# Optimization experiments

Hardware: AMD Instinct MI355X
Metric: run time of the kernel (lower is better)

## Reference

```python
import jax, jax.numpy as jnp
import numpy as np

EPSILON = 1e-5
N_ITER = 100  # module uses 100 iterations in eval mode (5 in training)
R = 0.01


def mdot(x, y):
    # Minkowski inner product with metric diag(-1, 1, ..., 1), reduced over dim 1.
    return jnp.sum(x * y, axis=1, keepdims=True) - 2.0 * x[:, :1] * y[:, :1]


def mnorm(x):
    return jnp.sqrt(jnp.abs(mdot(x, x)))


def arccosh(x):
    x = jnp.clip(x, 1.0 + EPSILON, None)
    return jnp.log(x) + jnp.log1p(jnp.sqrt(x * x - 1.0) / x)


def setup_inputs() -> dict:
    key = jax.random.key(0)
    data = jax.random.normal(key, (131072, 512), dtype=jnp.float32)
    return {"data": data}


def reference(data):
    # project onto hyperboloid: time coordinate sqrt(1 + |x|^2)
    t = jnp.sqrt(1.0 + jnp.sum(data * data, axis=1, keepdims=True))
    projected = jnp.concatenate([t, data], axis=1)  # [N, d+1]

    mean = jnp.mean(projected, axis=0, keepdims=True)  # [1, d+1]
    mean = mean / mnorm(mean)

    def step(mean, _):
        # log_map(mean, projected), broadcasting mean over N
        d = arccosh(-mdot(mean, projected))               # [N, 1]
        logm = d / jnp.sinh(d) * (projected - jnp.cosh(d) * mean)  # [N, d+1]
        g = -2.0 * jnp.mean(logm, axis=0, keepdims=True)  # [1, d+1]
        y = -R * g
        n = jnp.clip(mnorm(y), EPSILON, None)
        mean = jnp.cosh(n) * mean + jnp.sinh(n) / n * y   # exp_map
        mean = mean / mnorm(mean)
        return mean, None

    mean, _ = jax.lax.scan(step, mean, None, length=N_ITER)
    return jnp.squeeze(mean)[1:]  # drop time coordinate -> [d]
```

## Files before the change

### kernel.cpp

```cpp
#include <hip/hip_runtime.h>
#include <hip/hip_fp16.h>
#include <math.h>
#include <cstddef>

#define N_PTS 131072
#define SDIM  512
#define D1    513

static constexpr int NITER = 100;
static constexpr int BLK   = 512;
static constexpr int GRID  = 512;
static constexpr int WPB   = BLK / 64;
static constexpr int NW    = GRID * WPB;
static constexpr int NPAIR = N_PTS / 2;
static constexpr int PPW   = NPAIR / NW;

struct Ws {
  double colsum[514];
  double part[514][GRID];
  float  meanbuf[2][516];
  float  t_tab[N_PTS];
};

__device__ __forceinline__ float2 cvt2(unsigned u) {
  union { unsigned u; __half2 h; } c; c.u = u; return __half22float2(c.h);
}
__device__ __forceinline__ unsigned pack2(float a, float b) {
  union { unsigned u; __half2 h; } c; c.h = __floats2half2_rn(a, b); return c.u;
}

template<bool INIT>
__device__ __forceinline__ void compute_mean(const Ws* __restrict__ ws,
                                             const float* __restrict__ mprev,
                                             int l, float out[9])
{
  double sv[9];
  #pragma unroll
  for (int q = 0; q < 9; ++q) {
    int c = q * 64 + l;
    sv[q] = (c < D1) ? ws->colsum[c] : 0.0;
  }

  if constexpr (INIT) {
    double r[9]; double s2 = 0.0;
    #pragma unroll
    for (int q = 0; q < 9; ++q) {
      int c = q * 64 + l;
      r[q] = (c < D1) ? sv[q] / (double)N_PTS : 0.0;
      s2 += r[q] * r[q];
    }
    #pragma unroll
    for (int m = 1; m < 64; m <<= 1) s2 += __shfl_xor(s2, m);
    double rt = __shfl(r[8], 0);
    double inv = 1.0 / sqrt(fabs(s2 - 2.0 * rt * rt));
    #pragma unroll
    for (int q = 0; q < 9; ++q) out[q] = (float)(r[q] * inv);
  } else {
    double cc = ws->colsum[513];
    double mv[9], yv[9]; double sy = 0.0;
    #pragma unroll
    for (int q = 0; q < 9; ++q) {
      int c = q * 64 + l;
      mv[q] = 0.0; yv[q] = 0.0;
      if (c < D1) {
        double m = (double)mprev[c];
        double y = 0.02 * (sv[q] - cc * m) / (double)N_PTS;
        mv[q] = m; yv[q] = y;
        sy += y * y;
      }
    }
    #pragma unroll
    for (int m = 1; m < 64; m <<= 1) sy += __shfl_xor(sy, m);
    double yt = __shfl(yv[8], 0);
    double n = sqrt(fabs(sy - 2.0 * yt * yt));
    n = fmax(n, 1e-5);
    double ch = cosh(n);
    double sn = (n < 1e-4) ? (1.0 + n * n / 6.0) : (sinh(n) / n);
    double nm[9]; double s2 = 0.0;
    #pragma unroll
    for (int q = 0; q < 9; ++q) {
      nm[q] = ch * mv[q] + sn * yv[q];
      s2 += nm[q] * nm[q];
    }
    #pragma unroll
    for (int m = 1; m < 64; m <<= 1) s2 += __shfl_xor(s2, m);
    double nt = __shfl(nm[8], 0);
    double inv = 1.0 / sqrt(fabs(s2 - 2.0 * nt * nt));
    #pragma unroll
    for (int q = 0; q < 9; ++q) out[q] = (float)(nm[q] * inv);
  }
}

__global__ __launch_bounds__(BLK, 4)
void init_kernel(const float* __restrict__ data, __half* __restrict__ hdata,
                 Ws* __restrict__ ws)
{
  const int l    = threadIdx.x & 63;
  const int sl   = l & 31;
  const int half = l >> 5;
  const int wid  = threadIdx.x >> 6;
  const int gw   = blockIdx.x * WPB + wid;

  float accf[16] = {};
  double acc_t = 0.0;

  const int p0 = gw * PPW;

  float4 v0, v1, v2, v3, n0, n1, n2, n3;
  {
    const float4* f4 = (const float4*)(data + (size_t)(2 * p0 + half) * SDIM);
    v0 = f4[2*sl]; v1 = f4[2*sl+1]; v2 = f4[64+2*sl]; v3 = f4[64+2*sl+1];
  }

  for (int k = 0; k < PPW; ++k) {
    if (k + 1 < PPW) {
      const float4* f4 = (const float4*)(data + (size_t)(2 * (p0 + k + 1) + half) * SDIM);
      n0 = f4[2*sl]; n1 = f4[2*sl+1]; n2 = f4[64+2*sl]; n3 = f4[64+2*sl+1];
    } else { n0 = v0; n1 = v1; n2 = v2; n3 = v3; }

    const int row = 2 * (p0 + k) + half;

    {
      uint4 ua, ub;
      ua.x = pack2(v0.x, v0.y); ua.y = pack2(v0.z, v0.w);
      ua.z = pack2(v1.x, v1.y); ua.w = pack2(v1.z, v1.w);
      ub.x = pack2(v2.x, v2.y); ub.y = pack2(v2.z, v2.w);
      ub.z = pack2(v3.x, v3.y); ub.w = pack2(v3.z, v3.w);
      uint4* hb = (uint4*)(hdata + (size_t)row * SDIM);
      hb[sl] = ua; hb[32 + sl] = ub;
    }

    float sqa = v0.x * v0.x;
    sqa = fmaf(v0.y, v0.y, sqa); sqa = fmaf(v0.z, v0.z, sqa); sqa = fmaf(v0.w, v0.w, sqa);
    sqa = fmaf(v1.x, v1.x, sqa); sqa = fmaf(v1.y, v1.y, sqa);
    sqa = fmaf(v1.z, v1.z, sqa); sqa = fmaf(v1.w, v1.w, sqa);
    float sqb = v2.x * v2.x;
    sqb = fmaf(v2.y, v2.y, sqb); sqb = fmaf(v2.z, v2.z, sqb); sqb = fmaf(v2.w, v2.w, sqb);
    sqb = fmaf(v3.x, v3.x, sqb); sqb = fmaf(v3.y, v3.y, sqb);
    sqb = fmaf(v3.z, v3.z, sqb); sqb = fmaf(v3.w, v3.w, sqb);
    float sq = sqa + sqb;
    #pragma unroll
    for (int m = 1; m < 32; m <<= 1) sq += __shfl_xor(sq, m);

    float t = sqrtf(1.0f + sq);
    if (sl == 0) { ws->t_tab[row] = t; acc_t += (double)t; }

    accf[0]  += v0.x; accf[1]  += v0.y; accf[2]  += v0.z; accf[3]  += v0.w;
    accf[4]  += v1.x; accf[5]  += v1.y; accf[6]  += v1.z; accf[7]  += v1.w;
    accf[8]  += v2.x; accf[9]  += v2.y; accf[10] += v2.z; accf[11] += v2.w;
    accf[12] += v3.x; accf[13] += v3.y; accf[14] += v3.z; accf[15] += v3.w;

    v0 = n0; v1 = n1; v2 = n2; v3 = n3;
  }

  #pragma unroll
  for (int i = 0; i < 16; ++i) accf[i] += __shfl_xor(accf[i], 32);
  acc_t += __shfl_xor(acc_t, 32);

  __shared__ double s_red[WPB][514];
  if (half == 0) {
    #pragma unroll
    for (int i = 0; i < 8; ++i) {
      s_red[wid][8*sl + i]       = (double)accf[i];
      s_red[wid][256 + 8*sl + i] = (double)accf[8 + i];
    }
  }
  if (l == 0) { s_red[wid][512] = acc_t; s_red[wid][513] = 0.0; }
  __syncthreads();

  for (int c = threadIdx.x; c < 514; c += BLK) {
    double s = 0.0;
    #pragma unroll
    for (int w2 = 0; w2 < WPB; ++w2) s += s_red[w2][c];
    ws->part[c][blockIdx.x] = s;
  }
}

template<bool FIRST>
__global__ __launch_bounds__(BLK, 4)
void iter_kernel(const __half* __restrict__ hdata, Ws* __restrict__ ws,
                 const float* __restrict__ mprev, float* __restrict__ mnext)
{
  const int l    = threadIdx.x & 63;
  const int sl   = l & 31;
  const int half = l >> 5;
  const int wid  = threadIdx.x >> 6;
  const int gw   = blockIdx.x * WPB + wid;

  const int p0 = gw * PPW;

#define LDH(Ra, Rb, p) do {                                                   \
    const uint4* b_ = (const uint4*)(hdata + (size_t)(2 * (p) + half) * SDIM);\
    Ra = b_[sl]; Rb = b_[32 + sl];                                            \
  } while (0)

  uint4 Aa, Ab, Ba, Bb, Pa, Pb, Qa, Qb, Ra, Rb, Sa, Sb;
  LDH(Aa, Ab, p0 + 0);
  LDH(Ba, Bb, p0 + 1);

  __shared__ __align__(16) float s_mean[516];
  if (threadIdx.x < 64) {
    float outm[9];
    compute_mean<FIRST>(ws, mprev, threadIdx.x, outm);
    #pragma unroll
    for (int q = 0; q < 9; ++q) {
      int c = q * 64 + threadIdx.x;
      if (c < D1) {
        s_mean[c] = outm[q];
        if (blockIdx.x == 0) mnext[c] = outm[q];
      }
    }
  }
  __syncthreads();

  const float m0 = s_mean[512];
  const float4* mp4 = (const float4*)s_mean;
  const float4 mkA0 = mp4[2*sl],      mkA1 = mp4[2*sl + 1];
  const float4 mkB0 = mp4[64 + 2*sl], mkB1 = mp4[64 + 2*sl + 1];

  float accf[16] = {};
  double acc_t = 0.0, acc_cc = 0.0;
  const float* __restrict__ ttab = ws->t_tab;

  LDH(Pa, Pb, p0 + 2);
  LDH(Qa, Qb, p0 + 3);
  Ra = Aa; Rb = Ab; Sa = Ba; Sb = Bb;

  for (int kk = 0; kk < PPW; kk += 2) {
    if (kk + 4 < PPW) {
      LDH(Ra, Rb, p0 + kk + 4);
      LDH(Sa, Sb, p0 + kk + 5);
    }
    const float tA = ttab[2 * (p0 + kk)     + half];
    const float tB = ttab[2 * (p0 + kk + 1) + half];

    float2 f;
    f = cvt2(Aa.x); float dA  = f.x * mkA0.x;        dA  = fmaf(f.y, mkA0.y, dA);
    f = cvt2(Aa.y); dA  = fmaf(f.x, mkA0.z, dA);     dA  = fmaf(f.y, mkA0.w, dA);
    f = cvt2(Aa.z); dA  = fmaf(f.x, mkA1.x, dA);     dA  = fmaf(f.y, mkA1.y, dA);
    f = cvt2(Aa.w); dA  = fmaf(f.x, mkA1.z, dA);     dA  = fmaf(f.y, mkA1.w, dA);
    f = cvt2(Ab.x); float dA2 = f.x * mkB0.x;        dA2 = fmaf(f.y, mkB0.y, dA2);
    f = cvt2(Ab.y); dA2 = fmaf(f.x, mkB0.z, dA2);    dA2 = fmaf(f.y, mkB0.w, dA2);
    f = cvt2(Ab.z); dA2 = fmaf(f.x, mkB1.x, dA2);    dA2 = fmaf(f.y, mkB1.y, dA2);
    f = cvt2(Ab.w); dA2 = fmaf(f.x, mkB1.z, dA2);    dA2 = fmaf(f.y, mkB1.w, dA2);
    float dotA = dA + dA2;

    f = cvt2(Ba.x); float dB  = f.x * mkA0.x;        dB  = fmaf(f.y, mkA0.y, dB);
    f = cvt2(Ba.y); dB  = fmaf(f.x, mkA0.z, dB);     dB  = fmaf(f.y, mkA0.w, dB);
    f = cvt2(Ba.z); dB  = fmaf(f.x, mkA1.x, dB);     dB  = fmaf(f.y, mkA1.y, dB);
    f = cvt2(Ba.w); dB  = fmaf(f.x, mkA1.z, dB);     dB  = fmaf(f.y, mkA1.w, dB);
    f = cvt2(Bb.x); float dB2 = f.x * mkB0.x;        dB2 = fmaf(f.y, mkB0.y, dB2);
    f = cvt2(Bb.y); dB2 = fmaf(f.x, mkB0.z, dB2);    dB2 = fmaf(f.y, mkB0.w, dB2);
    f = cvt2(Bb.z); dB2 = fmaf(f.x, mkB1.x, dB2);    dB2 = fmaf(f.y, mkB1.y, dB2);
    f = cvt2(Bb.w); dB2 = fmaf(f.x, mkB1.z, dB2);    dB2 = fmaf(f.y, mkB1.w, dB2);
    float dotB = dB + dB2;

    #pragma unroll
    for (int m = 1; m < 32; m <<= 1) {
      dotA += __shfl_xor(dotA, m);
      dotB += __shfl_xor(dotB, m);
    }

    const float aA = fmaf(m0, tA, -dotA);
    const float aB = fmaf(m0, tB, -dotB);
    const float xA = fmaxf(aA, 1.0f + 1e-5f);
    const float xB = fmaxf(aB, 1.0f + 1e-5f);
    const float sA = sqrtf(fmaf(xA, xA, -1.0f));
    const float sB = sqrtf(fmaf(xB, xB, -1.0f));
    const float ddA = logf(xA + sA);
    const float ddB = logf(xB + sB);
    const float wA = ddA / sA;
    const float wB = ddB / sB;
    if (sl == 0) {
      acc_cc += fma((double)wA, (double)xA, (double)wB * (double)xB);
      acc_t  += fma((double)wA, (double)tA, (double)wB * (double)tB);
    }

    float2 a0, a1;
    a0 = cvt2(Aa.x); a1 = cvt2(Ba.x);
    accf[0]  = fmaf(wA, a0.x, fmaf(wB, a1.x, accf[0]));
    accf[1]  = fmaf(wA, a0.y, fmaf(wB, a1.y, accf[1]));
    a0 = cvt2(Aa.y); a1 = cvt2(Ba.y);
    accf[2]  = fmaf(wA, a0.x, fmaf(wB, a1.x, accf[2]));
    accf[3]  = fmaf(wA, a0.y, fmaf(wB, a1.y, accf[3]));
    a0 = cvt2(Aa.z); a1 = cvt2(Ba.z);
    accf[4]  = fmaf(wA, a0.x, fmaf(wB, a1.x, accf[4]));
    accf[5]  = fmaf(wA, a0.y, fmaf(wB, a1.y, accf[5]));
    a0 = cvt2(Aa.w); a1 = cvt2(Ba.w);
    accf[6]  = fmaf(wA, a0.x, fmaf(wB, a1.x, accf[6]));
    accf[7]  = fmaf(wA, a0.y, fmaf(wB, a1.y, accf[7]));
    a0 = cvt2(Ab.x); a1 = cvt2(Bb.x);
    accf[8]  = fmaf(wA, a0.x, fmaf(wB, a1.x, accf[8]));
    accf[9]  = fmaf(wA, a0.y, fmaf(wB, a1.y, accf[9]));
    a0 = cvt2(Ab.y); a1 = cvt2(Bb.y);
    accf[10] = fmaf(wA, a0.x, fmaf(wB, a1.x, accf[10]));
    accf[11] = fmaf(wA, a0.y, fmaf(wB, a1.y, accf[11]));
    a0 = cvt2(Ab.z); a1 = cvt2(Bb.z);
    accf[12] = fmaf(wA, a0.x, fmaf(wB, a1.x, accf[12]));
    accf[13] = fmaf(wA, a0.y, fmaf(wB, a1.y, accf[13]));
    a0 = cvt2(Ab.w); a1 = cvt2(Bb.w);
    accf[14] = fmaf(wA, a0.x, fmaf(wB, a1.x, accf[14]));
    accf[15] = fmaf(wA, a0.y, fmaf(wB, a1.y, accf[15]));

    Aa = Pa; Ab = Pb; Ba = Qa; Bb = Qb;
    Pa = Ra; Pb = Rb; Qa = Sa; Qb = Sb;
  }
#undef LDH

  #pragma unroll
  for (int i = 0; i < 16; ++i) accf[i] += __shfl_xor(accf[i], 32);
  acc_t  += __shfl_xor(acc_t, 32);
  acc_cc += __shfl_xor(acc_cc, 32);

  __shared__ double s_red[WPB][514];
  if (half == 0) {
    #pragma unroll
    for (int i = 0; i < 8; ++i) {
      s_red[wid][8*sl + i]       = (double)accf[i];
      s_red[wid][256 + 8*sl + i] = (double)accf[8 + i];
    }
  }
  if (l == 0) { s_red[wid][512] = acc_t; s_red[wid][513] = acc_cc; }
  __syncthreads();

  for (int c = threadIdx.x; c < 514; c += BLK) {
    double s = 0.0;
    #pragma unroll
    for (int w2 = 0; w2 < WPB; ++w2) s += s_red[w2][c];
    ws->part[c][blockIdx.x] = s;
  }
}

__global__ __launch_bounds__(64)
void colreduce_kernel(Ws* __restrict__ ws)
{
  const int c = blockIdx.x;
  const int l = threadIdx.x;
  const double* col = ws->part[c];
  double s = 0.0;
  #pragma unroll
  for (int k = 0; k < GRID / 64; ++k) s += col[l + 64 * k];
  #pragma unroll
  for (int m = 1; m < 64; m <<= 1) s += __shfl_xor(s, m);
  if (l == 0) ws->colsum[c] = s;
}

__global__ __launch_bounds__(64)
void final_kernel(Ws* __restrict__ ws, const float* __restrict__ mprev,
                  float* __restrict__ mnext)
{
  float outm[9];
  compute_mean<false>(ws, mprev, threadIdx.x, outm);
  #pragma unroll
  for (int q = 0; q < 9; ++q) {
    int c = q * 64 + threadIdx.x;
    if (c < D1) mnext[c] = outm[q];
  }
}

__global__ void write_out_kernel(const float* __restrict__ mean, float* __restrict__ out)
{
  int i = threadIdx.x;
  if (i < SDIM) out[i] = mean[i];
}

extern "C" void kernel_launch(void* const* d_in, const int* in_sizes, int n_in,
                              void* d_out, int out_size, void* d_ws, size_t ws_size,
                              hipStream_t stream)
{
  (void)in_sizes; (void)n_in; (void)out_size; (void)ws_size;
  const float* data = (const float*)d_in[0];
  Ws* ws = (Ws*)d_ws;

  const size_t hoff = (sizeof(Ws) + 255) & ~(size_t)255;
  __half* hdata = (__half*)((char*)d_ws + hoff);

  float* M0 = (float*)((char*)d_ws + offsetof(Ws, meanbuf));
  float* M1 = M0 + 516;

  init_kernel<<<dim3(GRID), dim3(BLK), 0, stream>>>(data, hdata, ws);
  colreduce_kernel<<<dim3(514), dim3(64), 0, stream>>>(ws);

  iter_kernel<true><<<dim3(GRID), dim3(BLK), 0, stream>>>(hdata, ws, M1, M0);
  colreduce_kernel<<<dim3(514), dim3(64), 0, stream>>>(ws);

  for (int it = 1; it < NITER; ++it) {
    const float* mp = (((it + 1) & 1) == 0) ? M0 : M1;
    float*       mn = ((it & 1) == 0) ? M0 : M1;
    iter_kernel<false><<<dim3(GRID), dim3(BLK), 0, stream>>>(hdata, ws, mp, mn);
    colreduce_kernel<<<dim3(514), dim3(64), 0, stream>>>(ws);
  }

  final_kernel<<<dim3(1), dim3(64), 0, stream>>>(ws, M1, M0);
  write_out_kernel<<<dim3(1), dim3(512), 0, stream>>>(M0, (float*)d_out);
}
```

Before: 3.180 ms.

## Store points as custom 8-bit floats and re-center weights around a constant

```diff
diff --git a/kernel.cpp b/kernel.cpp
--- a/kernel.cpp
+++ b/kernel.cpp
@@ -6,6 +6,7 @@
 #define N_PTS 131072
 #define SDIM  512
 #define D1    513
+#define W0F   0.169f
 
 static constexpr int NITER = 100;
 static constexpr int BLK   = 512;
@@ -17,16 +18,37 @@
 
 struct Ws {
   double colsum[514];
+  double X[514];
   double part[514][GRID];
   float  meanbuf[2][516];
   float  t_tab[N_PTS];
 };
 
-__device__ __forceinline__ float2 cvt2(unsigned u) {
-  union { unsigned u; __half2 h; } c; c.u = u; return __half22float2(c.h);
-}
-__device__ __forceinline__ unsigned pack2(float a, float b) {
-  union { unsigned u; __half2 h; } c; c.h = __floats2half2_rn(a, b); return c.u;
+__device__ __forceinline__ unsigned enc8(float x) {
+  unsigned u  = __float_as_uint(x);
+  unsigned s  = (u >> 24) & 0x80u;
+  unsigned au = u & 0x7fffffffu;
+  if (au < 0x3c800000u) return s;
+  unsigned r = au + 0x0007ffffu + ((au >> 20) & 1u);
+  unsigned e = r >> 23;
+  unsigned m = (r >> 20) & 7u;
+  if (e > 135u || (e == 135u && m > 6u)) return s | 0x7Eu;
+  return s | ((e - 120u) << 3) | m;
+}
+
+__device__ __forceinline__ unsigned dec8h(unsigned b) {
+  unsigned h = ((b & 0x80u) << 8) | ((b & 0x7fu) << 7);
+  return (b & 0x7fu) ? (h + 0x2000u) : h;
+}
+__device__ __forceinline__ float2 dec2(unsigned b0, unsigned b1) {
+  union { unsigned u; __half2 h; } c;
+  c.u = dec8h(b0) | (dec8h(b1) << 16);
+  return __half22float2(c.h);
+}
+__device__ __forceinline__ float4 dec4(unsigned v) {
+  float2 lo = dec2(v & 0xffu, (v >> 8) & 0xffu);
+  float2 hi = dec2((v >> 16) & 0xffu, v >> 24);
+  return make_float4(lo.x, lo.y, hi.x, hi.y);
 }
 
 template<bool INIT>
@@ -34,19 +56,12 @@
                                              const float* __restrict__ mprev,
                                              int l, float out[9])
 {
-  double sv[9];
-  #pragma unroll
-  for (int q = 0; q < 9; ++q) {
-    int c = q * 64 + l;
-    sv[q] = (c < D1) ? ws->colsum[c] : 0.0;
-  }
-
   if constexpr (INIT) {
     double r[9]; double s2 = 0.0;
     #pragma unroll
     for (int q = 0; q < 9; ++q) {
       int c = q * 64 + l;
-      r[q] = (c < D1) ? sv[q] / (double)N_PTS : 0.0;
+      r[q] = (c < D1) ? ws->colsum[c] / (double)N_PTS : 0.0;
       s2 += r[q] * r[q];
     }
     #pragma unroll
@@ -56,7 +71,28 @@
     #pragma unroll
     for (int q = 0; q < 9; ++q) out[q] = (float)(r[q] * inv);
   } else {
-    double cc = ws->colsum[513];
+    const double W0d = (double)W0F;
+    double xdm = 0.0;
+    #pragma unroll
+    for (int q = 0; q < 8; ++q) {
+      int c = q * 64 + l;
+      xdm += ws->X[c] * (double)mprev[c];
+    }
+    #pragma unroll
+    for (int m = 1; m < 64; m <<= 1) xdm += __shfl_xor(xdm, m);
+    const double T   = ws->X[512];
+    const double m0p = (double)mprev[512];
+
+    double sv[9];
+    #pragma unroll
+    for (int q = 0; q < 9; ++q) {
+      int c = q * 64 + l;
+      if (c < 512)       sv[q] = ws->colsum[c]   + W0d * ws->X[c];
+      else if (c == 512) sv[q] = ws->colsum[512] + W0d * T;
+      else               sv[q] = 0.0;
+    }
+    double cc = ws->colsum[513] + W0d * (m0p * T - xdm);
+
     double mv[9], yv[9]; double sy = 0.0;
     #pragma unroll
     for (int q = 0; q < 9; ++q) {
@@ -78,10 +114,7 @@
     double sn = (n < 1e-4) ? (1.0 + n * n / 6.0) : (sinh(n) / n);
     double nm[9]; double s2 = 0.0;
     #pragma unroll
-    for (int q = 0; q < 9; ++q) {
-      nm[q] = ch * mv[q] + sn * yv[q];
-      s2 += nm[q] * nm[q];
-    }
+    for (int q = 0; q < 9; ++q) { nm[q] = ch * mv[q] + sn * yv[q]; s2 += nm[q] * nm[q]; }
     #pragma unroll
     for (int m = 1; m < 64; m <<= 1) s2 += __shfl_xor(s2, m);
     double nt = __shfl(nm[8], 0);
@@ -92,7 +125,7 @@
 }
 
 __global__ __launch_bounds__(BLK, 4)
-void init_kernel(const float* __restrict__ data, __half* __restrict__ hdata,
+void init_kernel(const float* __restrict__ data, unsigned char* __restrict__ h8,
                  Ws* __restrict__ ws)
 {
   const int l    = threadIdx.x & 63;
@@ -103,7 +136,6 @@
 
   float accf[16] = {};
   double acc_t = 0.0;
-
   const int p0 = gw * PPW;
 
   float4 v0, v1, v2, v3, n0, n1, n2, n3;
@@ -121,13 +153,13 @@
     const int row = 2 * (p0 + k) + half;
 
     {
-      uint4 ua, ub;
-      ua.x = pack2(v0.x, v0.y); ua.y = pack2(v0.z, v0.w);
-      ua.z = pack2(v1.x, v1.y); ua.w = pack2(v1.z, v1.w);
-      ub.x = pack2(v2.x, v2.y); ub.y = pack2(v2.z, v2.w);
-      ub.z = pack2(v3.x, v3.y); ub.w = pack2(v3.z, v3.w);
-      uint4* hb = (uint4*)(hdata + (size_t)row * SDIM);
-      hb[sl] = ua; hb[32 + sl] = ub;
+      uint2 pa, pb;
+      pa.x = enc8(v0.x) | (enc8(v0.y) << 8) | (enc8(v0.z) << 16) | (enc8(v0.w) << 24);
+      pa.y = enc8(v1.x) | (enc8(v1.y) << 8) | (enc8(v1.z) << 16) | (enc8(v1.w) << 24);
+      pb.x = enc8(v2.x) | (enc8(v2.y) << 8) | (enc8(v2.z) << 16) | (enc8(v2.w) << 24);
+      pb.y = enc8(v3.x) | (enc8(v3.y) << 8) | (enc8(v3.z) << 16) | (enc8(v3.w) << 24);
+      uint2* hb = (uint2*)(h8 + (size_t)row * SDIM);
+      hb[sl] = pa; hb[32 + sl] = pb;
     }
 
     float sqa = v0.x * v0.x;
@@ -178,7 +210,7 @@
 
 template<bool FIRST>
 __global__ __launch_bounds__(BLK, 4)
-void iter_kernel(const __half* __restrict__ hdata, Ws* __restrict__ ws,
+void iter_kernel(const unsigned char* __restrict__ h8, Ws* __restrict__ ws,
                  const float* __restrict__ mprev, float* __restrict__ mnext)
 {
   const int l    = threadIdx.x & 63;
@@ -186,17 +218,16 @@
   const int half = l >> 5;
   const int wid  = threadIdx.x >> 6;
   const int gw   = blockIdx.x * WPB + wid;
-
-  const int p0 = gw * PPW;
-
-#define LDH(Ra, Rb, p) do {                                                   \
-    const uint4* b_ = (const uint4*)(hdata + (size_t)(2 * (p) + half) * SDIM);\
-    Ra = b_[sl]; Rb = b_[32 + sl];                                            \
+  const int p0   = gw * PPW;
+
+#define LDH8(R, p) do {                                                        \
+    const uint4* b_ = (const uint4*)(h8 + (size_t)(2 * (p) + half) * SDIM);    \
+    R = b_[sl];                                                                \
   } while (0)
 
-  uint4 Aa, Ab, Ba, Bb, Pa, Pb, Qa, Qb, Ra, Rb, Sa, Sb;
-  LDH(Aa, Ab, p0 + 0);
-  LDH(Ba, Bb, p0 + 1);
+  uint4 Aa, Ba, Pa, Qa, Ua, Va;
+  LDH8(Aa, p0 + 0);
+  LDH8(Ba, p0 + 1);
 
   __shared__ __align__(16) float s_mean[516];
   if (threadIdx.x < 64) {
@@ -215,44 +246,46 @@
 
   const float m0 = s_mean[512];
   const float4* mp4 = (const float4*)s_mean;
-  const float4 mkA0 = mp4[2*sl],      mkA1 = mp4[2*sl + 1];
-  const float4 mkB0 = mp4[64 + 2*sl], mkB1 = mp4[64 + 2*sl + 1];
+  const float4 mk0 = mp4[4*sl + 0], mk1 = mp4[4*sl + 1];
+  const float4 mk2 = mp4[4*sl + 2], mk3 = mp4[4*sl + 3];
 
   float accf[16] = {};
   double acc_t = 0.0, acc_cc = 0.0;
   const float* __restrict__ ttab = ws->t_tab;
 
-  LDH(Pa, Pb, p0 + 2);
-  LDH(Qa, Qb, p0 + 3);
-  Ra = Aa; Rb = Ab; Sa = Ba; Sb = Bb;
+  LDH8(Pa, p0 + 2);
+  LDH8(Qa, p0 + 3);
+  Ua = Aa; Va = Ba;
 
   for (int kk = 0; kk < PPW; kk += 2) {
     if (kk + 4 < PPW) {
-      LDH(Ra, Rb, p0 + kk + 4);
-      LDH(Sa, Sb, p0 + kk + 5);
+      LDH8(Ua, p0 + kk + 4);
+      LDH8(Va, p0 + kk + 5);
     }
     const float tA = ttab[2 * (p0 + kk)     + half];
     const float tB = ttab[2 * (p0 + kk + 1) + half];
 
-    float2 f;
-    f = cvt2(Aa.x); float dA  = f.x * mkA0.x;        dA  = fmaf(f.y, mkA0.y, dA);
-    f = cvt2(Aa.y); dA  = fmaf(f.x, mkA0.z, dA);     dA  = fmaf(f.y, mkA0.w, dA);
-    f = cvt2(Aa.z); dA  = fmaf(f.x, mkA1.x, dA);     dA  = fmaf(f.y, mkA1.y, dA);
-    f = cvt2(Aa.w); dA  = fmaf(f.x, mkA1.z, dA);     dA  = fmaf(f.y, mkA1.w, dA);
-    f = cvt2(Ab.x); float dA2 = f.x * mkB0.x;        dA2 = fmaf(f.y, mkB0.y, dA2);
-    f = cvt2(Ab.y); dA2 = fmaf(f.x, mkB0.z, dA2);    dA2 = fmaf(f.y, mkB0.w, dA2);
-    f = cvt2(Ab.z); dA2 = fmaf(f.x, mkB1.x, dA2);    dA2 = fmaf(f.y, mkB1.y, dA2);
-    f = cvt2(Ab.w); dA2 = fmaf(f.x, mkB1.z, dA2);    dA2 = fmaf(f.y, mkB1.w, dA2);
+    float4 a0 = dec4(Aa.x), a1 = dec4(Aa.y), a2 = dec4(Aa.z), a3 = dec4(Aa.w);
+    float4 b0 = dec4(Ba.x), b1 = dec4(Ba.y), b2 = dec4(Ba.z), b3 = dec4(Ba.w);
+
+    float dA = a0.x * mk0.x;
+    dA = fmaf(a0.y, mk0.y, dA); dA = fmaf(a0.z, mk0.z, dA); dA = fmaf(a0.w, mk0.w, dA);
+    dA = fmaf(a1.x, mk1.x, dA); dA = fmaf(a1.y, mk1.y, dA);
+    dA = fmaf(a1.z, mk1.z, dA); dA = fmaf(a1.w, mk1.w, dA);
+    float dA2 = a2.x * mk2.x;
+    dA2 = fmaf(a2.y, mk2.y, dA2); dA2 = fmaf(a2.z, mk2.z, dA2); dA2 = fmaf(a2.w, mk2.w, dA2);
+    dA2 = fmaf(a3.x, mk3.x, dA2); dA2 = fmaf(a3.y, mk3.y, dA2);
+    dA2 = fmaf(a3.z, mk3.z, dA2); dA2 = fmaf(a3.w, mk3.w, dA2);
     float dotA = dA + dA2;
 
-    f = cvt2(Ba.x); float dB  = f.x * mkA0.x;        dB  = fmaf(f.y, mkA0.y, dB);
-    f = cvt2(Ba.y); dB  = fmaf(f.x, mkA0.z, dB);     dB  = fmaf(f.y, mkA0.w, dB);
-    f = cvt2(Ba.z); dB  = fmaf(f.x, mkA1.x, dB);     dB  = fmaf(f.y, mkA1.y, dB);
-    f = cvt2(Ba.w); dB  = fmaf(f.x, mkA1.z, dB);     dB  = fmaf(f.y, mkA1.w, dB);
-    f = cvt2(Bb.x); float dB2 = f.x * mkB0.x;        dB2 = fmaf(f.y, mkB0.y, dB2);
-    f = cvt2(Bb.y); dB2 = fmaf(f.x, mkB0.z, dB2);    dB2 = fmaf(f.y, mkB0.w, dB2);
-    f = cvt2(Bb.z); dB2 = fmaf(f.x, mkB1.x, dB2);    dB2 = fmaf(f.y, mkB1.y, dB2);
-    f = cvt2(Bb.w); dB2 = fmaf(f.x, mkB1.z, dB2);    dB2 = fmaf(f.y, mkB1.w, dB2);
+    float dB = b0.x * mk0.x;
+    dB = fmaf(b0.y, mk0.y, dB); dB = fmaf(b0.z, mk0.z, dB); dB = fmaf(b0.w, mk0.w, dB);
+    dB = fmaf(b1.x, mk1.x, dB); dB = fmaf(b1.y, mk1.y, dB);
+    dB = fmaf(b1.z, mk1.z, dB); dB = fmaf(b1.w, mk1.w, dB);
+    float dB2 = b2.x * mk2.x;
+    dB2 = fmaf(b2.y, mk2.y, dB2); dB2 = fmaf(b2.z, mk2.z, dB2); dB2 = fmaf(b2.w, mk2.w, dB2);
+    dB2 = fmaf(b3.x, mk3.x, dB2); dB2 = fmaf(b3.y, mk3.y, dB2);
+    dB2 = fmaf(b3.z, mk3.z, dB2); dB2 = fmaf(b3.w, mk3.w, dB2);
     float dotB = dB + dB2;
 
     #pragma unroll
@@ -267,45 +300,36 @@
     const float xB = fmaxf(aB, 1.0f + 1e-5f);
     const float sA = sqrtf(fmaf(xA, xA, -1.0f));
     const float sB = sqrtf(fmaf(xB, xB, -1.0f));
-    const float ddA = logf(xA + sA);
-    const float ddB = logf(xB + sB);
-    const float wA = ddA / sA;
-    const float wB = ddB / sB;
+    const float wA = logf(xA + sA) / sA;
+    const float wB = logf(xB + sB) / sB;
+    const float cA = wA - W0F;
+    const float cB = wB - W0F;
     if (sl == 0) {
-      acc_cc += fma((double)wA, (double)xA, (double)wB * (double)xB);
-      acc_t  += fma((double)wA, (double)tA, (double)wB * (double)tB);
-    }
-
-    float2 a0, a1;
-    a0 = cvt2(Aa.x); a1 = cvt2(Ba.x);
-    accf[0]  = fmaf(wA, a0.x, fmaf(wB, a1.x, accf[0]));
-    accf[1]  = fmaf(wA, a0.y, fmaf(wB, a1.y, accf[1]));
-    a0 = cvt2(Aa.y); a1 = cvt2(Ba.y);
-    accf[2]  = fmaf(wA, a0.x, fmaf(wB, a1.x, accf[2]));
-    accf[3]  = fmaf(wA, a0.y, fmaf(wB, a1.y, accf[3]));
-    a0 = cvt2(Aa.z); a1 = cvt2(Ba.z);
-    accf[4]  = fmaf(wA, a0.x, fmaf(wB, a1.x, accf[4]));
-    accf[5]  = fmaf(wA, a0.y, fmaf(wB, a1.y, accf[5]));
-    a0 = cvt2(Aa.w); a1 = cvt2(Ba.w);
-    accf[6]  = fmaf(wA, a0.x, fmaf(wB, a1.x, accf[6]));
-    accf[7]  = fmaf(wA, a0.y, fmaf(wB, a1.y, accf[7]));
-    a0 = cvt2(Ab.x); a1 = cvt2(Bb.x);
-    accf[8]  = fmaf(wA, a0.x, fmaf(wB, a1.x, accf[8]));
-    accf[9]  = fmaf(wA, a0.y, fmaf(wB, a1.y, accf[9]));
-    a0 = cvt2(Ab.y); a1 = cvt2(Bb.y);
-    accf[10] = fmaf(wA, a0.x, fmaf(wB, a1.x, accf[10]));
-    accf[11] = fmaf(wA, a0.y, fmaf(wB, a1.y, accf[11]));
-    a0 = cvt2(Ab.z); a1 = cvt2(Bb.z);
-    accf[12] = fmaf(wA, a0.x, fmaf(wB, a1.x, accf[12]));
-    accf[13] = fmaf(wA, a0.y, fmaf(wB, a1.y, accf[13]));
-    a0 = cvt2(Ab.w); a1 = cvt2(Bb.w);
-    accf[14] = fmaf(wA, a0.x, fmaf(wB, a1.x, accf[14]));
-    accf[15] = fmaf(wA, a0.y, fmaf(wB, a1.y, accf[15]));
-
-    Aa = Pa; Ab = Pb; Ba = Qa; Bb = Qb;
-    Pa = Ra; Pb = Rb; Qa = Sa; Qb = Sb;
-  }
-#undef LDH
+      acc_cc += fma((double)cA, (double)xA, (double)cB * (double)xB);
+      acc_t  += fma((double)cA, (double)tA, (double)cB * (double)tB);
+    }
+
+    accf[0]  = fmaf(cA, a0.x, fmaf(cB, b0.x, accf[0]));
+    accf[1]  = fmaf(cA, a0.y, fmaf(cB, b0.y, accf[1]));
+    accf[2]  = fmaf(cA, a0.z, fmaf(cB, b0.z, accf[2]));
+    accf[3]  = fmaf(cA, a0.w, fmaf(cB, b0.w, accf[3]));
+    accf[4]  = fmaf(cA, a1.x, fmaf(cB, b1.x, accf[4]));
+    accf[5]  = fmaf(cA, a1.y, fmaf(cB, b1.y, accf[5]));
+    accf[6]  = fmaf(cA, a1.z, fmaf(cB, b1.z, accf[6]));
+    accf[7]  = fmaf(cA, a1.w, fmaf(cB, b1.w, accf[7]));
+    accf[8]  = fmaf(cA, a2.x, fmaf(cB, b2.x, accf[8]));
+    accf[9]  = fmaf(cA, a2.y, fmaf(cB, b2.y, accf[9]));
+    accf[10] = fmaf(cA, a2.z, fmaf(cB, b2.z, accf[10]));
+    accf[11] = fmaf(cA, a2.w, fmaf(cB, b2.w, accf[11]));
+    accf[12] = fmaf(cA, a3.x, fmaf(cB, b3.x, accf[12]));
+    accf[13] = fmaf(cA, a3.y, fmaf(cB, b3.y, accf[13]));
+    accf[14] = fmaf(cA, a3.z, fmaf(cB, b3.z, accf[14]));
+    accf[15] = fmaf(cA, a3.w, fmaf(cB, b3.w, accf[15]));
+
+    Aa = Pa; Ba = Qa;
+    Pa = Ua; Qa = Va;
+  }
+#undef LDH8
 
   #pragma unroll
   for (int i = 0; i < 16; ++i) accf[i] += __shfl_xor(accf[i], 32);
@@ -315,10 +339,7 @@
   __shared__ double s_red[WPB][514];
   if (half == 0) {
     #pragma unroll
-    for (int i = 0; i < 8; ++i) {
-      s_red[wid][8*sl + i]       = (double)accf[i];
-      s_red[wid][256 + 8*sl + i] = (double)accf[8 + i];
-    }
+    for (int i = 0; i < 16; ++i) s_red[wid][16*sl + i] = (double)accf[i];
   }
   if (l == 0) { s_red[wid][512] = acc_t; s_red[wid][513] = acc_cc; }
   __syncthreads();
@@ -331,6 +352,7 @@
   }
 }
 
+template<bool WRITE_X>
 __global__ __launch_bounds__(64)
 void colreduce_kernel(Ws* __restrict__ ws)
 {
@@ -342,7 +364,10 @@
   for (int k = 0; k < GRID / 64; ++k) s += col[l + 64 * k];
   #pragma unroll
   for (int m = 1; m < 64; m <<= 1) s += __shfl_xor(s, m);
-  if (l == 0) ws->colsum[c] = s;
+  if (l == 0) {
+    ws->colsum[c] = s;
+    if constexpr (WRITE_X) ws->X[c] = s;
+  }
 }
 
 __global__ __launch_bounds__(64)
@@ -373,22 +398,22 @@
   Ws* ws = (Ws*)d_ws;
 
   const size_t hoff = (sizeof(Ws) + 255) & ~(size_t)255;
-  __half* hdata = (__half*)((char*)d_ws + hoff);
+  unsigned char* h8 = (unsigned char*)d_ws + hoff;
 
   float* M0 = (float*)((char*)d_ws + offsetof(Ws, meanbuf));
   float* M1 = M0 + 516;
 
-  init_kernel<<<dim3(GRID), dim3(BLK), 0, stream>>>(data, hdata, ws);
-  colreduce_kernel<<<dim3(514), dim3(64), 0, stream>>>(ws);
-
-  iter_kernel<true><<<dim3(GRID), dim3(BLK), 0, stream>>>(hdata, ws, M1, M0);
-  colreduce_kernel<<<dim3(514), dim3(64), 0, stream>>>(ws);
+  init_kernel<<<dim3(GRID), dim3(BLK), 0, stream>>>(data, h8, ws);
+  colreduce_kernel<true><<<dim3(514), dim3(64), 0, stream>>>(ws);
+
+  iter_kernel<true><<<dim3(GRID), dim3(BLK), 0, stream>>>(h8, ws, M1, M0);
+  colreduce_kernel<false><<<dim3(514), dim3(64), 0, stream>>>(ws);
 
   for (int it = 1; it < NITER; ++it) {
     const float* mp = (((it + 1) & 1) == 0) ? M0 : M1;
     float*       mn = ((it & 1) == 0) ? M0 : M1;
-    iter_kernel<false><<<dim3(GRID), dim3(BLK), 0, stream>>>(hdata, ws, mp, mn);
-    colreduce_kernel<<<dim3(514), dim3(64), 0, stream>>>(ws);
+    iter_kernel<false><<<dim3(GRID), dim3(BLK), 0, stream>>>(h8, ws, mp, mn);
+    colreduce_kernel<false><<<dim3(514), dim3(64), 0, stream>>>(ws);
   }
 
   final_kernel<<<dim3(1), dim3(64), 0, stream>>>(ws, M1, M0);
```

Result: slower. 3.429 ms (+7.8%).
